# Kernel optimization log

Hardware: AMD Instinct MI355X
Metric: run time of the kernel (lower is better)

## Reference

```python
import jax, jax.numpy as jnp
import numpy as np

N_GROUP, D, DFF = 8, 256, 1024
T = 131072  # total routed tokens


def setup_inputs() -> dict:
    key = jax.random.key(0)
    k_x, k_g, k_u, k_d = jax.random.split(key, 4)
    # kaiming_uniform_(a=sqrt(5)) over fan_in == second-to-last dim
    def kaiming(k, shape, fan_in):
        bound = 1.0 / np.sqrt(fan_in)
        return jax.random.uniform(k, shape, jnp.float32, -bound, bound)
    x = jax.random.normal(k_x, (T, D), jnp.float32)
    weight_gate = kaiming(k_g, (N_GROUP, D, DFF), D)
    weight_up = kaiming(k_u, (N_GROUP, D, DFF), D)
    weight_down = kaiming(k_d, (N_GROUP, DFF, D), DFF)
    # cumulative group end offsets; uniform groups of T // N_GROUP tokens
    offs = (jnp.arange(1, N_GROUP + 1, dtype=jnp.int32) * (T // N_GROUP))
    return {"x": x, "weight_gate": weight_gate, "weight_up": weight_up,
            "weight_down": weight_down, "offs": offs}


def reference(x, weight_gate, weight_up, weight_down, offs):
    # Grouped GLU: for tokens in group g, y = silu(x @ Wg_gate) * (x @ Wg_up) @ Wg_down.
    # offs encodes uniform group boundaries (offs[i] = (i+1)*T/G), so the grouped
    # GEMM is a batched matmul over the expert axis after a reshape.
    G = weight_gate.shape[0]
    t, d = x.shape
    xg = x.reshape(G, t // G, d)                                  # [G, Tg, d]
    z_gate = jnp.einsum('gtd,gdf->gtf', xg, weight_gate)          # [G, Tg, dff]
    z_up = jnp.einsum('gtd,gdf->gtf', xg, weight_up)
    h = jax.nn.silu(z_gate) * z_up
    y = jnp.einsum('gtf,gfd->gtd', h, weight_down)                # [G, Tg, d]
    return y.reshape(t, d)
```

## Files before the change

kernel.cpp:

```cpp
#include <hip/hip_runtime.h>

typedef __bf16 bf16x8 __attribute__((ext_vector_type(8)));
typedef float f32x16 __attribute__((ext_vector_type(16)));
typedef unsigned int u32x4 __attribute__((ext_vector_type(4)));

#define NGROUP 8
#define DMODEL 256
#define DFF    1024
#define TTOT   131072
#define TGRP   (TTOT / NGROUP)
#define MTILE  256
#define NCHUNK 32

__device__ __forceinline__ unsigned int f2bf(float f) {
    unsigned int x = __builtin_bit_cast(unsigned int, f);
    return (x + 0x7fffu + ((x >> 16) & 1u)) >> 16;
}
__device__ __forceinline__ unsigned int pack2(float lo, float hi) {
    return f2bf(lo) | (f2bf(hi) << 16);
}

__device__ __forceinline__ void g2l(const void* g, void* l) {
    __builtin_amdgcn_global_load_lds(
        (const __attribute__((address_space(1))) unsigned int*)g,
        (__attribute__((address_space(3))) unsigned int*)l, 16, 0, 0);
}

__global__ void k_cvt_x(const float4* __restrict__ in, u32x4* __restrict__ out) {
    int t = blockIdx.x * 256 + threadIdx.x;
    float4 a = in[2 * t];
    float4 b = in[2 * t + 1];
    u32x4 v = { pack2(a.x, a.y), pack2(a.z, a.w), pack2(b.x, b.y), pack2(b.z, b.w) };
    out[t] = v;
}

__global__ void k_prep_w(const float* __restrict__ wg, const float* __restrict__ wu,
                         const float* __restrict__ wd, u32x4* __restrict__ out) {
    int t = blockIdx.x * 256 + threadIdx.x;
    int lane = t & 63;
    int q = lane >> 5, l31 = lane & 31;
    int fg = t >> 6;
    int fid = fg % 48;
    int gc  = fg / 48;
    int c = gc & 31, g = gc >> 5;
    const float* src;
    int stride;
    if (fid < 32) {
        const float* w = (fid < 16) ? wg : wu;
        int ks = fid & 15;
        src = w + (size_t)(g * 256 + ks * 16 + q * 8) * 1024 + c * 32 + l31;
        stride = 1024;
    } else {
        int idx = fid - 32;
        int ks2 = idx >> 3, nb = idx & 7;
        src = wd + (size_t)(g * 1024 + (c * 2 + ks2) * 16 + q * 8) * 256 + nb * 32 + l31;
        stride = 256;
    }
    u32x4 v = { pack2(src[0],          src[stride]),
                pack2(src[2 * stride], src[3 * stride]),
                pack2(src[4 * stride], src[5 * stride]),
                pack2(src[6 * stride], src[7 * stride]) };
    out[t] = v;
}

__global__ __launch_bounds__(512, 2)
void k_glu(const u32x4* __restrict__ xb,
           const u32x4* __restrict__ wcomb,
           float* __restrict__ y) {
    __shared__ u32x4 smem[4096];

    const int tid  = threadIdx.x;
    const int lane = tid & 63;
    const int w    = tid >> 6;
    const int q    = lane >> 5;
    const int l31  = lane & 31;

    const int g    = blockIdx.x & 7;
    const int m0   = g * TGRP + (blockIdx.x >> 3) * MTILE;
    const int tokw = w * 32 + l31;

    u32x4 xf[16];
    {
        const u32x4* xrow = xb + (size_t)(m0 + tokw) * 32 + q;
        #pragma unroll
        for (int ks = 0; ks < 16; ++ks) xf[ks] = xrow[ks * 2];
    }

    f32x16 acc[8];
    #pragma unroll
    for (int nb = 0; nb < 8; ++nb)
        #pragma unroll
        for (int i = 0; i < 16; ++i) acc[nb][i] = 0.0f;

    const u32x4* wcg = wcomb + (size_t)(g * 32) * 3072;
    const unsigned int sw = ((l31 >> 2) & 3) << 4;
    char* hrow = (char*)smem + 49152 + w * 2048 + l31 * 64;

    for (int c = 0; c < NCHUNK; ++c) {
        __syncthreads();
        {
            const u32x4* gsrc = wcg + (size_t)c * 3072;
            #pragma unroll
            for (int i = 0; i < 6; ++i) {
                int off = i * 512 + w * 64;
                g2l(gsrc + off + lane, smem + off);
            }
        }
        __syncthreads();

        f32x16 zg, zu;
        #pragma unroll
        for (int i = 0; i < 16; ++i) { zg[i] = 0.0f; zu[i] = 0.0f; }
        #pragma unroll
        for (int ks = 0; ks < 16; ++ks) {
            const u32x4 a1 = smem[ks * 64 + lane];
            const u32x4 a2 = smem[1024 + ks * 64 + lane];
            zg = __builtin_amdgcn_mfma_f32_32x32x16_bf16(
                     __builtin_bit_cast(bf16x8, a1),
                     __builtin_bit_cast(bf16x8, xf[ks]), zg, 0, 0, 0);
            zu = __builtin_amdgcn_mfma_f32_32x32x16_bf16(
                     __builtin_bit_cast(bf16x8, a2),
                     __builtin_bit_cast(bf16x8, xf[ks]), zu, 0, 0, 0);
        }

        #pragma unroll
        for (int a = 0; a < 4; ++a) {
            const float g0 = zg[4 * a + 0], g1 = zg[4 * a + 1];
            const float g2 = zg[4 * a + 2], g3 = zg[4 * a + 3];
            const float h0 = g0 / (1.0f + __expf(-g0)) * zu[4 * a + 0];
            const float h1 = g1 / (1.0f + __expf(-g1)) * zu[4 * a + 1];
            const float h2 = g2 / (1.0f + __expf(-g2)) * zu[4 * a + 2];
            const float h3 = g3 / (1.0f + __expf(-g3)) * zu[4 * a + 3];
            uint2 pv;
            pv.x = pack2(h0, h1);
            pv.y = pack2(h2, h3);
            *(uint2*)(hrow + ((unsigned)(a * 16 + q * 8) ^ sw)) = pv;
        }

        #pragma unroll
        for (int ks2 = 0; ks2 < 2; ++ks2) {
            const u32x4 ha = *(const u32x4*)(hrow + ((unsigned)(ks2 * 32 + q * 16) ^ sw));
            #pragma unroll
            for (int nb = 0; nb < 8; ++nb) {
                const u32x4 bd = smem[2048 + (ks2 * 8 + nb) * 64 + lane];
                acc[nb] = __builtin_amdgcn_mfma_f32_32x32x16_bf16(
                              __builtin_bit_cast(bf16x8, ha),
                              __builtin_bit_cast(bf16x8, bd), acc[nb], 0, 0, 0);
            }
        }
    }

    float* yp = y + (size_t)(m0 + w * 32) * DMODEL;
    #pragma unroll
    for (int nb = 0; nb < 8; ++nb) {
        const int col = nb * 32 + l31;
        #pragma unroll
        for (int r = 0; r < 16; ++r) {
            const int row = (r & 3) + (r >> 2) * 8 + q * 4;
            yp[(size_t)row * DMODEL + col] = acc[nb][r];
        }
    }
}

extern "C" void kernel_launch(void* const* d_in, const int* in_sizes, int n_in,
                              void* d_out, int out_size, void* d_ws, size_t ws_size,
                              hipStream_t stream) {
    const float* x  = (const float*)d_in[0];
    const float* wg = (const float*)d_in[1];
    const float* wu = (const float*)d_in[2];
    const float* wd = (const float*)d_in[3];
    float* y = (float*)d_out;

    u32x4* xb    = (u32x4*)d_ws;
    u32x4* wcomb = xb + 4194304;

    k_cvt_x<<<dim3(TTOT * DMODEL / 8 / 256), dim3(256), 0, stream>>>((const float4*)x, xb);
    k_prep_w<<<dim3(3072), dim3(256), 0, stream>>>(wg, wu, wd, wcomb);
    k_glu<<<dim3(512), dim3(512), 0, stream>>>(xb, wcomb, y);
}
```

Baseline: 485.2 us.

## Fuse x conversion into GLU kernel, double-buffer weight chunks, keep h in registers

Drops the separate x fp32-to-bf16 conversion kernel and its workspace round trip; x is now loaded as fp32 and packed to bf16 in-register with v_cvt_pk_bf16_f32. Weight chunks are double-buffered in LDS, so the next chunk's global_load_lds runs while the current chunk computes, with explicit waitcnt and barriers. The down-projection weight layout is permuted so the MFMA accumulator output of the gate/up GEMM can feed the down GEMM directly as the A operand, which removes the LDS store and reload of h. Side changes add s_setprio around MFMA bursts and use rcp in place of division in SiLU. LDS use grows to 96KB, which may limit occupancy.

```diff
diff --git a/kernel.cpp b/kernel.cpp
--- a/kernel.cpp
+++ b/kernel.cpp
@@ -19,19 +19,16 @@
 __device__ __forceinline__ unsigned int pack2(float lo, float hi) {
     return f2bf(lo) | (f2bf(hi) << 16);
 }
+__device__ __forceinline__ unsigned int cvtpk(float lo, float hi) {
+    unsigned int r;
+    asm("v_cvt_pk_bf16_f32 %0, %1, %2" : "=v"(r) : "v"(lo), "v"(hi));
+    return r;
+}
 
 __device__ __forceinline__ void g2l(const void* g, void* l) {
     __builtin_amdgcn_global_load_lds(
         (const __attribute__((address_space(1))) unsigned int*)g,
         (__attribute__((address_space(3))) unsigned int*)l, 16, 0, 0);
-}
-
-__global__ void k_cvt_x(const float4* __restrict__ in, u32x4* __restrict__ out) {
-    int t = blockIdx.x * 256 + threadIdx.x;
-    float4 a = in[2 * t];
-    float4 b = in[2 * t + 1];
-    u32x4 v = { pack2(a.x, a.y), pack2(a.z, a.w), pack2(b.x, b.y), pack2(b.z, b.w) };
-    out[t] = v;
 }
 
 __global__ void k_prep_w(const float* __restrict__ wg, const float* __restrict__ wu,
@@ -43,31 +40,32 @@
     int fid = fg % 48;
     int gc  = fg / 48;
     int c = gc & 31, g = gc >> 5;
-    const float* src;
-    int stride;
+    u32x4 v;
     if (fid < 32) {
         const float* w = (fid < 16) ? wg : wu;
         int ks = fid & 15;
-        src = w + (size_t)(g * 256 + ks * 16 + q * 8) * 1024 + c * 32 + l31;
-        stride = 1024;
+        const float* src = w + (size_t)(g * 256 + ks * 16 + q * 8) * 1024 + c * 32 + l31;
+        v = u32x4{ pack2(src[0],        src[1024]),
+                   pack2(src[2 * 1024], src[3 * 1024]),
+                   pack2(src[4 * 1024], src[5 * 1024]),
+                   pack2(src[6 * 1024], src[7 * 1024]) };
     } else {
         int idx = fid - 32;
         int ks2 = idx >> 3, nb = idx & 7;
-        src = wd + (size_t)(g * 1024 + (c * 2 + ks2) * 16 + q * 8) * 256 + nb * 32 + l31;
-        stride = 256;
-    }
-    u32x4 v = { pack2(src[0],          src[stride]),
-                pack2(src[2 * stride], src[3 * stride]),
-                pack2(src[4 * stride], src[5 * stride]),
-                pack2(src[6 * stride], src[7 * stride]) };
+        const float* src = wd + (size_t)(g * 1024 + c * 32 + ks2 * 16 + q * 4) * 256 + nb * 32 + l31;
+        v = u32x4{ pack2(src[0 * 256],  src[1 * 256]),
+                   pack2(src[2 * 256],  src[3 * 256]),
+                   pack2(src[8 * 256],  src[9 * 256]),
+                   pack2(src[10 * 256], src[11 * 256]) };
+    }
     out[t] = v;
 }
 
 __global__ __launch_bounds__(512, 2)
-void k_glu(const u32x4* __restrict__ xb,
+void k_glu(const float* __restrict__ x,
            const u32x4* __restrict__ wcomb,
            float* __restrict__ y) {
-    __shared__ u32x4 smem[4096];
+    __shared__ u32x4 smem[6144];
 
     const int tid  = threadIdx.x;
     const int lane = tid & 63;
@@ -77,13 +75,27 @@
 
     const int g    = blockIdx.x & 7;
     const int m0   = g * TGRP + (blockIdx.x >> 3) * MTILE;
-    const int tokw = w * 32 + l31;
-
+    const int tok  = m0 + w * 32 + l31;
+
+    const u32x4* wcg = wcomb + (size_t)(g * 32) * 3072;
+
+    {
+        #pragma unroll
+        for (int i = 0; i < 6; ++i) {
+            int off = i * 512 + w * 64;
+            g2l(wcg + off + lane, smem + off);
+        }
+    }
     u32x4 xf[16];
     {
-        const u32x4* xrow = xb + (size_t)(m0 + tokw) * 32 + q;
-        #pragma unroll
-        for (int ks = 0; ks < 16; ++ks) xf[ks] = xrow[ks * 2];
+        const float* xrow = x + (size_t)tok * DMODEL + q * 8;
+        #pragma unroll
+        for (int ks = 0; ks < 16; ++ks) {
+            float4 a = *(const float4*)(xrow + ks * 16);
+            float4 b = *(const float4*)(xrow + ks * 16 + 4);
+            xf[ks] = u32x4{ cvtpk(a.x, a.y), cvtpk(a.z, a.w),
+                            cvtpk(b.x, b.y), cvtpk(b.z, b.w) };
+        }
     }
 
     f32x16 acc[8];
@@ -92,29 +104,36 @@
         #pragma unroll
         for (int i = 0; i < 16; ++i) acc[nb][i] = 0.0f;
 
-    const u32x4* wcg = wcomb + (size_t)(g * 32) * 3072;
-    const unsigned int sw = ((l31 >> 2) & 3) << 4;
-    char* hrow = (char*)smem + 49152 + w * 2048 + l31 * 64;
+    asm volatile("s_waitcnt vmcnt(0)" ::: "memory");
+    __builtin_amdgcn_s_barrier();
+    asm volatile("" ::: "memory");
 
     for (int c = 0; c < NCHUNK; ++c) {
-        __syncthreads();
-        {
-            const u32x4* gsrc = wcg + (size_t)c * 3072;
+        const u32x4* sb = smem + (c & 1) * 3072;
+
+        if (c + 1 < NCHUNK) {
+            u32x4* db = smem + ((c + 1) & 1) * 3072;
+            const u32x4* gsrc = wcg + (size_t)(c + 1) * 3072;
             #pragma unroll
             for (int i = 0; i < 6; ++i) {
                 int off = i * 512 + w * 64;
-                g2l(gsrc + off + lane, smem + off);
+                g2l(gsrc + off + lane, db + off);
             }
-        }
-        __syncthreads();
+            asm volatile("s_waitcnt vmcnt(6)" ::: "memory");
+        } else {
+            asm volatile("s_waitcnt vmcnt(0)" ::: "memory");
+        }
+        __builtin_amdgcn_s_barrier();
+        asm volatile("" ::: "memory");
 
         f32x16 zg, zu;
         #pragma unroll
         for (int i = 0; i < 16; ++i) { zg[i] = 0.0f; zu[i] = 0.0f; }
+        __builtin_amdgcn_s_setprio(1);
         #pragma unroll
         for (int ks = 0; ks < 16; ++ks) {
-            const u32x4 a1 = smem[ks * 64 + lane];
-            const u32x4 a2 = smem[1024 + ks * 64 + lane];
+            const u32x4 a1 = sb[ks * 64 + lane];
+            const u32x4 a2 = sb[1024 + ks * 64 + lane];
             zg = __builtin_amdgcn_mfma_f32_32x32x16_bf16(
                      __builtin_bit_cast(bf16x8, a1),
                      __builtin_bit_cast(bf16x8, xf[ks]), zg, 0, 0, 0);
@@ -122,32 +141,39 @@
                      __builtin_bit_cast(bf16x8, a2),
                      __builtin_bit_cast(bf16x8, xf[ks]), zu, 0, 0, 0);
         }
-
-        #pragma unroll
-        for (int a = 0; a < 4; ++a) {
-            const float g0 = zg[4 * a + 0], g1 = zg[4 * a + 1];
-            const float g2 = zg[4 * a + 2], g3 = zg[4 * a + 3];
-            const float h0 = g0 / (1.0f + __expf(-g0)) * zu[4 * a + 0];
-            const float h1 = g1 / (1.0f + __expf(-g1)) * zu[4 * a + 1];
-            const float h2 = g2 / (1.0f + __expf(-g2)) * zu[4 * a + 2];
-            const float h3 = g3 / (1.0f + __expf(-g3)) * zu[4 * a + 3];
-            uint2 pv;
-            pv.x = pack2(h0, h1);
-            pv.y = pack2(h2, h3);
-            *(uint2*)(hrow + ((unsigned)(a * 16 + q * 8) ^ sw)) = pv;
-        }
-
-        #pragma unroll
-        for (int ks2 = 0; ks2 < 2; ++ks2) {
-            const u32x4 ha = *(const u32x4*)(hrow + ((unsigned)(ks2 * 32 + q * 16) ^ sw));
-            #pragma unroll
-            for (int nb = 0; nb < 8; ++nb) {
-                const u32x4 bd = smem[2048 + (ks2 * 8 + nb) * 64 + lane];
-                acc[nb] = __builtin_amdgcn_mfma_f32_32x32x16_bf16(
-                              __builtin_bit_cast(bf16x8, ha),
-                              __builtin_bit_cast(bf16x8, bd), acc[nb], 0, 0, 0);
-            }
-        }
+        __builtin_amdgcn_s_setprio(0);
+
+        float hv[16];
+        #pragma unroll
+        for (int i = 0; i < 16; ++i) {
+            const float gv = zg[i];
+            const float s  = __builtin_amdgcn_rcpf(1.0f + __expf(-gv));
+            hv[i] = gv * s * zu[i];
+        }
+        const u32x4 ha0 = u32x4{ cvtpk(hv[0], hv[1]),   cvtpk(hv[2], hv[3]),
+                                 cvtpk(hv[4], hv[5]),   cvtpk(hv[6], hv[7]) };
+        const u32x4 ha1 = u32x4{ cvtpk(hv[8], hv[9]),   cvtpk(hv[10], hv[11]),
+                                 cvtpk(hv[12], hv[13]), cvtpk(hv[14], hv[15]) };
+        const bf16x8 A0 = __builtin_bit_cast(bf16x8, ha0);
+        const bf16x8 A1 = __builtin_bit_cast(bf16x8, ha1);
+
+        __builtin_amdgcn_s_setprio(1);
+        #pragma unroll
+        for (int nb = 0; nb < 8; ++nb) {
+            acc[nb] = __builtin_amdgcn_mfma_f32_32x32x16_bf16(
+                          A0, __builtin_bit_cast(bf16x8, sb[2048 + nb * 64 + lane]),
+                          acc[nb], 0, 0, 0);
+        }
+        #pragma unroll
+        for (int nb = 0; nb < 8; ++nb) {
+            acc[nb] = __builtin_amdgcn_mfma_f32_32x32x16_bf16(
+                          A1, __builtin_bit_cast(bf16x8, sb[2048 + (8 + nb) * 64 + lane]),
+                          acc[nb], 0, 0, 0);
+        }
+        __builtin_amdgcn_s_setprio(0);
+
+        asm volatile("" ::: "memory");
+        __builtin_amdgcn_s_barrier();
     }
 
     float* yp = y + (size_t)(m0 + w * 32) * DMODEL;
@@ -171,10 +197,8 @@
     const float* wd = (const float*)d_in[3];
     float* y = (float*)d_out;
 
-    u32x4* xb    = (u32x4*)d_ws;
-    u32x4* wcomb = xb + 4194304;
-
-    k_cvt_x<<<dim3(TTOT * DMODEL / 8 / 256), dim3(256), 0, stream>>>((const float4*)x, xb);
+    u32x4* wcomb = (u32x4*)d_ws;
+
     k_prep_w<<<dim3(3072), dim3(256), 0, stream>>>(wg, wu, wd, wcomb);
-    k_glu<<<dim3(512), dim3(512), 0, stream>>>(xb, wcomb, y);
-}
+    k_glu<<<dim3(512), dim3(512), 0, stream>>>(x, wcomb, y);
+}
```

After: 414.5 us. 14.6% less time.
